# Kernel tuning notes

Hardware: AMD Instinct MI355X
Metric: run time of the kernel (lower is better)

Reference implementation:

```python
import jax, jax.numpy as jnp
import numpy as np

N_E = 8192
E_DIM = 256
BETA = 0.25


def setup_inputs() -> dict:
    key = jax.random.key(0)
    k1, k2 = jax.random.split(key)
    z = jax.random.normal(k1, (16, E_DIM, 32, 32), dtype=jnp.float32)
    # torch init: uniform(-1/n_e, 1/n_e)
    emb_weight = jax.random.uniform(k2, (N_E, E_DIM), dtype=jnp.float32,
                                    minval=-1.0 / N_E, maxval=1.0 / N_E)
    return {"z": z, "emb_weight": emb_weight}


def reference(z, emb_weight):
    B, C, H, W = z.shape
    # NCHW -> NHWC, flatten to [N, e_dim]
    z_nhwc = jnp.transpose(z, (0, 2, 3, 1))
    zf = z_nhwc.reshape(-1, C)  # [N, e_dim]

    # squared euclidean distances: ||z||^2 + ||e||^2 - 2 z e^T  -> [N, n_e]
    d = (jnp.sum(zf * zf, axis=1, keepdims=True)
         + jnp.sum(emb_weight * emb_weight, axis=1)
         - 2.0 * jnp.matmul(zf, emb_weight.T))
    idx = jnp.argmin(d, axis=1)  # [N]

    z_q = emb_weight[idx].reshape(z_nhwc.shape)  # [B,H,W,C]

    # legacy loss: mean((sg(z_q)-z)^2) + beta*mean((z_q-sg(z))^2)
    sg = jax.lax.stop_gradient
    loss = (jnp.mean((sg(z_q) - z_nhwc) ** 2)
            + BETA * jnp.mean((z_q - sg(z_nhwc)) ** 2))

    # straight-through estimator
    z_q = z_nhwc + sg(z_q - z_nhwc)

    # perplexity via code-usage histogram (equivalent to mean of one-hot)
    counts = jnp.zeros((N_E,), dtype=z.dtype).at[idx].add(1.0)
    e_mean = counts / idx.shape[0]
    perplexity = jnp.exp(-jnp.sum(e_mean * jnp.log(e_mean + 1e-10)))

    min_encoding_indices = idx.reshape(B, H * W).astype(jnp.int32)

    z_q = jnp.transpose(z_q, (0, 3, 1, 2))  # back to NCHW
    return z_q, loss, perplexity, min_encoding_indices
```

## Files before the change

### kernel.cpp

```cpp
#include <hip/hip_runtime.h>
#include <math.h>

#define NPTS   16384
#define NE     8192
#define DIM    256
#define BIMG   16
#define HW     1024
#define ZQ_N   4194304
#define OFF_LOSS  4194304
#define OFF_PERP  4194305
#define OFF_IDX   4194306

#define NT     64
#define NUNITS (NPTS * NT)
#define SJCAP  1048576

typedef short s16x8 __attribute__((ext_vector_type(8)));
typedef float f32x4 __attribute__((ext_vector_type(4)));

__device__ __forceinline__ float mul_rn(float a, float b) {
    float r;
    asm("v_mul_f32 %0, %1, %2" : "=v"(r) : "v"(a), "v"(b));
    return r;
}

__device__ __forceinline__ unsigned short f2bf(float f) {
    unsigned int u = __float_as_uint(f);
    return (unsigned short)((u + 0x7fffu + ((u >> 16) & 1u)) >> 16);
}

__device__ __forceinline__ void gl_lds16(const void* g, void* l) {
    __builtin_amdgcn_global_load_lds(
        (const __attribute__((address_space(1))) void*)g,
        (__attribute__((address_space(3))) void*)l, 16, 0, 0);
}

__device__ __forceinline__ void dot_min(const float* __restrict__ zp,
                                        const float* __restrict__ e,
                                        float zq, int p, int c,
                                        unsigned long long* __restrict__ pbest) {
    const float4* zp4 = (const float4*)zp;
    const float4* ep = (const float4*)(e + (size_t)c * 256);
    float a = 0.f;
    for (int k4 = 0; k4 < 64; ++k4) {
        float4 zv = zp4[k4];
        float4 ev = ep[k4];
        a = fmaf(zv.x, ev.x, a);
        a = fmaf(zv.y, ev.y, a);
        a = fmaf(zv.z, ev.z, a);
        a = fmaf(zv.w, ev.w, a);
    }
    float d = zq - 2.0f * a;
    unsigned long long key =
        ((unsigned long long)__float_as_uint(d) << 32) | (unsigned int)c;
    atomicMin(pbest + p, key);
}

__global__ __launch_bounds__(256)
void k_prep_z(const float* __restrict__ z, float* __restrict__ zT,
              unsigned short* __restrict__ zhT) {
    int bid = blockIdx.x;
    int ht = bid & 15, kt = (bid >> 4) & 3, b = bid >> 6;
    int k0 = kt * 64, hw0 = ht * 64;
    __shared__ float lt[64][65];
    int t = threadIdx.x;
    {
        int kr = t >> 2, j4 = (t & 3) * 16;
        const float* src = z + ((size_t)b * 256 + k0 + kr) * 1024 + hw0 + j4;
        #pragma unroll
        for (int q = 0; q < 4; ++q) {
            float4 v = *(const float4*)(src + q * 4);
            lt[kr][j4 + q * 4 + 0] = v.x; lt[kr][j4 + q * 4 + 1] = v.y;
            lt[kr][j4 + q * 4 + 2] = v.z; lt[kr][j4 + q * 4 + 3] = v.w;
        }
    }
    __syncthreads();
    {
        int pr = t >> 2, kb = (t & 3) * 16;
        size_t p = (size_t)b * 1024 + hw0 + pr;
        float vals[16];
        #pragma unroll
        for (int i = 0; i < 16; ++i) vals[i] = lt[kb + i][pr];
        float* dst = zT + p * 256 + k0 + kb;
        #pragma unroll
        for (int q = 0; q < 4; ++q)
            *(float4*)(dst + q * 4) = make_float4(vals[q*4], vals[q*4+1],
                                                  vals[q*4+2], vals[q*4+3]);
        unsigned short* hd = zhT + p * 256 + k0 + kb;
        #pragma unroll
        for (int q = 0; q < 4; ++q) {
            ushort4 h;
            h.x = f2bf(vals[q*4]);   h.y = f2bf(vals[q*4+1]);
            h.z = f2bf(vals[q*4+2]); h.w = f2bf(vals[q*4+3]);
            *(ushort4*)(hd + q * 4) = h;
        }
    }
}

__global__ void k_prep_e(const float* __restrict__ e, unsigned short* __restrict__ eh) {
    size_t i = ((size_t)blockIdx.x * 256 + threadIdx.x) * 16;
    #pragma unroll
    for (int q = 0; q < 4; ++q) {
        float4 v = *(const float4*)(e + i + q * 4);
        ushort4 h;
        h.x = f2bf(v.x); h.y = f2bf(v.y); h.z = f2bf(v.z); h.w = f2bf(v.w);
        *(ushort4*)(eh + i + q * 4) = h;
    }
}

__global__ void k_zsq(const float* __restrict__ zT, float* __restrict__ zsq,
                      float* __restrict__ marg) {
    int gid = blockIdx.x * 256 + threadIdx.x;
    int P = gid >> 1, half = gid & 1;
    const float* row = zT + (size_t)P * 256 + half * 128;
    float r[8];
    float S = 0.f;
    #pragma unroll
    for (int j = 0; j < 8; ++j) {
        float v = row[j];
        r[j] = mul_rn(v, v);
        S += fabsf(v);
    }
    for (int i = 8; i < 128; i += 8)
        #pragma unroll
        for (int j = 0; j < 8; ++j) {
            float v = row[i + j];
            r[j] += mul_rn(v, v);
            S += fabsf(v);
        }
    float s = ((r[0] + r[1]) + (r[2] + r[3])) + ((r[4] + r[5]) + (r[6] + r[7]));
    float so = __shfl_xor(s, 1, 64);
    float So = __shfl_xor(S, 1, 64);
    if (half == 0) {
        float zq = s + so;
        zsq[P] = zq;
        float Stot = S + So;
        unsigned int bits = __float_as_uint(zq);
        int ex = (int)((bits >> 23) & 255);
        float q = __uint_as_float((unsigned int)(ex - 23) << 23);
        marg[P] = 0.5f * q + 9.6e-7f * Stot + 2e-6f;
    }
}

__global__ void k_init(int* __restrict__ hist,
                       unsigned long long* __restrict__ pbest,
                       int* __restrict__ jc, int* __restrict__ tcnt) {
    int i = blockIdx.x * 256 + threadIdx.x;
    if (i < NE) hist[i] = 0;
    pbest[i] = ~0ULL;
    if (i < 2) jc[i] = 0;
    if (i < NT) tcnt[i] = 0;
}

__global__ __launch_bounds__(256)
void k_gemm(const unsigned short* __restrict__ zhT,
            const unsigned short* __restrict__ eh,
            float* __restrict__ tileMax) {
    const int bid = blockIdx.x;
    const int bm = bid & 127;
    const int bn = bid >> 7;
    const int t = threadIdx.x;
    const int l = t & 63, w = t >> 6, wm = w >> 1, wn = w & 1;

    __shared__ unsigned short As[2][128 * 32];
    __shared__ unsigned short Bs[2][128 * 32];
    __shared__ float wred[2][128];

    const unsigned short* Ab = zhT + (size_t)(bm * 128) * 256;
    const unsigned short* Bb = eh + (size_t)(bn * 128) * 256;
    const int srow = t >> 2, sko = (t & 3) * 8;

    gl_lds16(Ab + (size_t)srow * 256 + sko,        &As[0][t * 8]);
    gl_lds16(Ab + (size_t)(srow + 64) * 256 + sko, &As[0][t * 8 + 2048]);
    gl_lds16(Bb + (size_t)srow * 256 + sko,        &Bs[0][t * 8]);
    gl_lds16(Bb + (size_t)(srow + 64) * 256 + sko, &Bs[0][t * 8 + 2048]);

    f32x4 acc[4][4];
    #pragma unroll
    for (int m = 0; m < 4; ++m)
        #pragma unroll
        for (int n = 0; n < 4; ++n)
            acc[m][n] = (f32x4){0.f, 0.f, 0.f, 0.f};

    const int r0 = wm * 64 + (l & 15);
    const int c0 = wn * 64 + (l & 15);
    const int ko = (l >> 4) * 8;

    int buf = 0;
    for (int kc = 0; kc < 8; ++kc) {
        __syncthreads();
        if (kc < 7) {
            int kk = (kc + 1) * 32;
            gl_lds16(Ab + (size_t)srow * 256 + kk + sko,        &As[buf ^ 1][t * 8]);
            gl_lds16(Ab + (size_t)(srow + 64) * 256 + kk + sko, &As[buf ^ 1][t * 8 + 2048]);
            gl_lds16(Bb + (size_t)srow * 256 + kk + sko,        &Bs[buf ^ 1][t * 8]);
            gl_lds16(Bb + (size_t)(srow + 64) * 256 + kk + sko, &Bs[buf ^ 1][t * 8 + 2048]);
        }
        s16x8 af[4], bfr[4];
        #pragma unroll
        for (int m = 0; m < 4; ++m)
            af[m] = *(const s16x8*)&As[buf][(r0 + m * 16) * 32 + ko];
        #pragma unroll
        for (int n = 0; n < 4; ++n)
            bfr[n] = *(const s16x8*)&Bs[buf][(c0 + n * 16) * 32 + ko];
        #pragma unroll
        for (int m = 0; m < 4; ++m)
            #pragma unroll
            for (int n = 0; n < 4; ++n)
                acc[m][n] = __builtin_amdgcn_mfma_f32_16x16x32_bf16(
                    af[m], bfr[n], acc[m][n], 0, 0, 0);
        __syncthreads();
        buf ^= 1;
    }

    float vmax[4][4];
    #pragma unroll
    for (int m = 0; m < 4; ++m)
        #pragma unroll
        for (int q = 0; q < 4; ++q) {
            float v = acc[m][0][q];
            v = fmaxf(v, acc[m][1][q]);
            v = fmaxf(v, acc[m][2][q]);
            v = fmaxf(v, acc[m][3][q]);
            vmax[m][q] = v;
        }
    #pragma unroll
    for (int m = 0; m < 4; ++m)
        #pragma unroll
        for (int q = 0; q < 4; ++q) {
            float v = vmax[m][q];
            #pragma unroll
            for (int msk = 1; msk < 16; msk <<= 1)
                v = fmaxf(v, __shfl_xor(v, msk, 64));
            vmax[m][q] = v;
        }
    if ((l & 15) == 0) {
        int rg = l >> 4;
        #pragma unroll
        for (int m = 0; m < 4; ++m)
            #pragma unroll
            for (int q = 0; q < 4; ++q)
                wred[wn][wm * 64 + m * 16 + rg * 4 + q] = vmax[m][q];
    }
    __syncthreads();
    if (t < 128)
        tileMax[(size_t)bn * NPTS + bm * 128 + t] =
            fmaxf(wred[0][t], wred[1][t]);
}

__global__ void k_flag(const float* __restrict__ tileMax,
                       const float* __restrict__ marg,
                       float* __restrict__ tau) {
    int p = blockIdx.x * 256 + threadIdx.x;
    float best = -1e30f;
    for (int T = 0; T < NT; ++T)
        best = fmaxf(best, tileMax[(size_t)T * NPTS + p]);
    tau[p] = best - marg[p];
}

__global__ __launch_bounds__(256)
void k_filter(const float* __restrict__ tileMax,
              const float* __restrict__ tau,
              int* __restrict__ flist, int* __restrict__ tcnt) {
    const int T = blockIdx.x >> 6;
    const int chunk = blockIdx.x & 63;
    const int t = threadIdx.x;
    const int p = chunk * 256 + t;
    __shared__ int lcnt, gbase;
    if (t == 0) lcnt = 0;
    __syncthreads();
    bool hit = tileMax[(size_t)T * NPTS + p] >= tau[p];
    int myoff = 0;
    if (hit) myoff = atomicAdd(&lcnt, 1);
    __syncthreads();
    if (t == 0) gbase = (lcnt > 0) ? atomicAdd(&tcnt[T], lcnt) : 0;
    __syncthreads();
    if (hit) flist[T * NPTS + gbase + myoff] = p;
}

__global__ void k_scan(const int* __restrict__ tcnt, int* __restrict__ soff) {
    __shared__ int s[65];
    int t = threadIdx.x;
    if (t < 64) s[t + 1] = (tcnt[t] + 127) >> 7;
    if (t == 0) s[0] = 0;
    __syncthreads();
    if (t == 0)
        for (int i = 1; i <= 64; ++i) s[i] += s[i - 1];
    __syncthreads();
    if (t <= 64) soff[t] = s[t];
}

__global__ __launch_bounds__(256)
void k_gemm2s(const unsigned short* __restrict__ zhT,
              const unsigned short* __restrict__ eh,
              const int* __restrict__ flist, const int* __restrict__ tcnt,
              const int* __restrict__ soff,
              const float* __restrict__ tau,
              unsigned int* __restrict__ jobs, int* __restrict__ jc,
              const float* __restrict__ zT, const float* __restrict__ e,
              const float* __restrict__ zsq,
              unsigned long long* __restrict__ pbest) {
    const int t = threadIdx.x;
    const int l = t & 63, w = t >> 6, wm = w >> 1, wn = w & 1;
    const int lx = l & 15;
    const int kg = l >> 4;
    const int ko = kg * 8;

    __shared__ int soff_s[65];
    __shared__ int pid_s[128];
    __shared__ float stau[128];
    __shared__ int lcnt, gbase;

    if (t < 65) soff_s[t] = soff[t];
    __syncthreads();
    const int totS = soff_s[64];

    for (int j = blockIdx.x; j < totS; j += gridDim.x) {
        int lo = 0, hi = 63;
        while (lo < hi) {
            int mid = (lo + hi + 1) >> 1;
            if (soff_s[mid] <= j) lo = mid; else hi = mid - 1;
        }
        const int T = lo, sl = j - soff_s[T], nf = tcnt[T];

        __syncthreads();
        if (t < 128) {
            int gi = sl * 128 + t;
            int p = (gi < nf) ? flist[T * NPTS + gi] : flist[T * NPTS];
            pid_s[t] = p;
            stau[t] = tau[p];
        }
        if (t == 0) lcnt = 0;
        __syncthreads();

        int prow[4];
        #pragma unroll
        for (int m = 0; m < 4; ++m) prow[m] = pid_s[wm * 64 + m * 16 + lx];

        f32x4 acc[4][4];
        #pragma unroll
        for (int m = 0; m < 4; ++m)
            #pragma unroll
            for (int n = 0; n < 4; ++n)
                acc[m][n] = (f32x4){0.f, 0.f, 0.f, 0.f};

        const unsigned short* Bb = eh + (size_t)(T * 128 + wn * 64 + lx) * 256;
        #pragma unroll 2
        for (int kc = 0; kc < 8; ++kc) {
            s16x8 af[4], bfr[4];
            #pragma unroll
            for (int m = 0; m < 4; ++m)
                af[m] = *(const s16x8*)(zhT + (size_t)prow[m] * 256 + kc * 32 + ko);
            #pragma unroll
            for (int n = 0; n < 4; ++n)
                bfr[n] = *(const s16x8*)(Bb + (size_t)(n * 16) * 256 + kc * 32 + ko);
            #pragma unroll
            for (int m = 0; m < 4; ++m)
                #pragma unroll
                for (int n = 0; n < 4; ++n)
                    acc[m][n] = __builtin_amdgcn_mfma_f32_16x16x32_bf16(
                        af[m], bfr[n], acc[m][n], 0, 0, 0);
        }

        int cnt = 0;
        #pragma unroll
        for (int m = 0; m < 4; ++m)
            #pragma unroll
            for (int q = 0; q < 4; ++q) {
                int row = wm * 64 + m * 16 + kg * 4 + q;
                float st = stau[row];
                #pragma unroll
                for (int n = 0; n < 4; ++n)
                    if (acc[m][n][q] >= st) ++cnt;
            }
        int myoff = 0;
        if (cnt) myoff = atomicAdd(&lcnt, cnt);
        __syncthreads();
        if (t == 0) gbase = (lcnt > 0) ? atomicAdd(jc, lcnt) : 0;
        __syncthreads();
        if (cnt) {
            int pos = gbase + myoff;
            #pragma unroll
            for (int m = 0; m < 4; ++m)
                #pragma unroll
                for (int q = 0; q < 4; ++q) {
                    int row = wm * 64 + m * 16 + kg * 4 + q;
                    float st = stau[row];
                    #pragma unroll
                    for (int n = 0; n < 4; ++n) {
                        if (acc[m][n][q] >= st) {
                            int p = pid_s[row];
                            int c = T * 128 + wn * 64 + n * 16 + lx;
                            if (pos < SJCAP)
                                jobs[pos] = ((unsigned int)p << 13) | (unsigned int)c;
                            else
                                dot_min(zT + (size_t)p * 256, e, zsq[p], p, c, pbest);
                            ++pos;
                        }
                    }
                }
        }
    }
}

__global__ __launch_bounds__(256)
void k_rescore(const unsigned int* __restrict__ jobs, const int* __restrict__ jc,
               const float* __restrict__ zT, const float* __restrict__ e,
               const float* __restrict__ zsq,
               unsigned long long* __restrict__ pbest) {
    int nS = jc[0]; if (nS > SJCAP) nS = SJCAP;
    int stride = gridDim.x * 256;
    for (int j = blockIdx.x * 256 + threadIdx.x; j < nS; j += stride) {
        unsigned int v = jobs[j];
        int p = (int)(v >> 13);
        int c = (int)(v & 8191u);
        dot_min(zT + (size_t)p * 256, e, zsq[p], p, c, pbest);
    }
}

__global__ void k_pick(const unsigned long long* __restrict__ pbest,
                       int* __restrict__ idx_i, int* __restrict__ hist,
                       float* __restrict__ out) {
    int P = blockIdx.x * 256 + threadIdx.x;
    unsigned long long key = pbest[P];
    int idx = (int)(unsigned int)(key & 0xffffffffULL);
    idx_i[P] = idx;
    out[OFF_IDX + P] = (float)idx;
    atomicAdd(&hist[idx], 1);
}

__global__ __launch_bounds__(256)
void k_gather(const float* __restrict__ z, const float* __restrict__ emb,
              const int* __restrict__ idx_i, float* __restrict__ out,
              float* __restrict__ partials) {
    int bid = blockIdx.x;
    int c = bid & 255;
    int b = bid >> 8;
    int t = threadIdx.x;
    int hw = t * 4;

    size_t zoff = (size_t)(b * DIM + c) * HW + hw;
    const float4 zv = *(const float4*)(z + zoff);
    const int4  iv = *(const int4*)(idx_i + b * HW + hw);

    float e0 = emb[(size_t)iv.x * DIM + c];
    float e1 = emb[(size_t)iv.y * DIM + c];
    float e2 = emb[(size_t)iv.z * DIM + c];
    float e3 = emb[(size_t)iv.w * DIM + c];

    float dx = e0 - zv.x, dy = e1 - zv.y, dz = e2 - zv.z, dw = e3 - zv.w;
    float4 ov = make_float4(zv.x + dx, zv.y + dy, zv.z + dz, zv.w + dw);
    *(float4*)(out + zoff) = ov;

    float sq = dx * dx + dy * dy + dz * dz + dw * dw;
    #pragma unroll
    for (int m = 32; m >= 1; m >>= 1) sq += __shfl_xor(sq, m, 64);
    __shared__ float red[4];
    if ((t & 63) == 0) red[t >> 6] = sq;
    __syncthreads();
    if (t == 0) partials[bid] = red[0] + red[1] + red[2] + red[3];
}

__global__ void k_final(const float* __restrict__ partials,
                        const int* __restrict__ hist,
                        float* __restrict__ out) {
    int t = threadIdx.x;
    double ls = 0.0, es = 0.0;
    for (int i = t; i < 4096; i += 256) ls += (double)partials[i];
    for (int i = t; i < NE; i += 256) {
        double em = (double)hist[i] / (double)NPTS;
        es += em * log(em + 1e-10);
    }
    __shared__ double s1[256], s2[256];
    s1[t] = ls; s2[t] = es;
    __syncthreads();
    for (int s = 128; s > 0; s >>= 1) {
        if (t < s) { s1[t] += s1[t + s]; s2[t] += s2[t + s]; }
        __syncthreads();
    }
    if (t == 0) {
        out[OFF_LOSS] = (float)(s1[0] / (double)ZQ_N * 1.25);
        out[OFF_PERP] = (float)exp(-s2[0]);
    }
}

__global__ void f_zsq(const float* __restrict__ z, float* __restrict__ zsq) {
    int gid = blockIdx.x * 256 + threadIdx.x;
    int P = gid >> 1, half = gid & 1;
    int b = P >> 10, hw = P & 1023;
    const float* zb = z + (size_t)b * (DIM * HW) + (size_t)(half * 128) * HW + hw;
    float r[8];
    #pragma unroll
    for (int j = 0; j < 8; ++j) {
        float v = zb[(size_t)j * HW];
        r[j] = mul_rn(v, v);
    }
    #pragma unroll
    for (int i = 8; i < 128; i += 8)
        #pragma unroll
        for (int j = 0; j < 8; ++j) {
            float v = zb[(size_t)(i + j) * HW];
            r[j] += mul_rn(v, v);
        }
    float s = ((r[0] + r[1]) + (r[2] + r[3])) + ((r[4] + r[5]) + (r[6] + r[7]));
    float o = __shfl_xor(s, 1, 64);
    if (half == 0) zsq[P] = s + o;
}

__global__ void f_init(int* __restrict__ hist) {
    hist[blockIdx.x * 256 + threadIdx.x] = 0;
}

#define FBP 64
#define FBC 256
#define FKC 32
__global__ __launch_bounds__(256, 2)
void f_argmin(const float* __restrict__ z, const float* __restrict__ emb,
              const float* __restrict__ zsq,
              float* __restrict__ cand_d, int* __restrict__ cand_c) {
    const int blk = blockIdx.x;
    const int pblk = blk & 255;
    const int split = blk >> 8;
    const int p0 = pblk * FBP;
    const int b = p0 >> 10;
    const int hw0 = p0 & 1023;
    const int t = threadIdx.x;
    const int tx = t & 31;
    const int ty = t >> 5;

    __shared__ __align__(16) float z_s[FBP][36];
    __shared__ __align__(16) float e_s[FBC][36];

    float bd[8];
    int bcn[8];
    #pragma unroll
    for (int i = 0; i < 8; ++i) { bd[i] = INFINITY; bcn[i] = 0x7fffffff; }
    float zsqv[8];
    #pragma unroll
    for (int i = 0; i < 8; ++i) zsqv[i] = zsq[p0 + ty * 8 + i];

    const float* zbase = z + (size_t)b * (DIM * HW) + hw0;

    for (int cc = split * 16; cc < (split + 1) * 16; ++cc) {
        float acc[8][8];
        #pragma unroll
        for (int i = 0; i < 8; ++i)
            #pragma unroll
            for (int j = 0; j < 8; ++j) acc[i][j] = 0.f;
        for (int kc = 0; kc < DIM / FKC; ++kc) {
            __syncthreads();
            {
                int i = t & 63, kk0 = t >> 6;
                #pragma unroll
                for (int r = 0; r < 8; ++r) {
                    int kk = kk0 + r * 4;
                    z_s[i][kk] = zbase[(size_t)(kc * FKC + kk) * HW + i];
                }
            }
            {
                #pragma unroll
                for (int it = 0; it < 8; ++it) {
                    int q = t + it * 256;
                    int r = q >> 3, kkq = q & 7;
                    const float4 v = *(const float4*)(emb +
                        (size_t)(cc * FBC + r) * DIM + kc * FKC + kkq * 4);
                    *(float4*)&e_s[r][kkq * 4] = v;
                }
            }
            __syncthreads();
            #pragma unroll
            for (int g = 0; g < 8; ++g) {
                float4 zf[8], ef[8];
                #pragma unroll
                for (int i = 0; i < 8; ++i)
                    zf[i] = *(const float4*)&z_s[ty * 8 + i][g * 4];
                #pragma unroll
                for (int j = 0; j < 8; ++j)
                    ef[j] = *(const float4*)&e_s[tx + j * 32][g * 4];
                #pragma unroll
                for (int i = 0; i < 8; ++i)
                    #pragma unroll
                    for (int j = 0; j < 8; ++j) {
                        float a = acc[i][j];
                        a = fmaf(zf[i].x, ef[j].x, a);
                        a = fmaf(zf[i].y, ef[j].y, a);
                        a = fmaf(zf[i].z, ef[j].z, a);
                        a = fmaf(zf[i].w, ef[j].w, a);
                        acc[i][j] = a;
                    }
            }
        }
        #pragma unroll
        for (int j = 0; j < 8; ++j) {
            int c = cc * FBC + tx + j * 32;
            #pragma unroll
            for (int i = 0; i < 8; ++i) {
                float d = zsqv[i] - 2.0f * acc[i][j];
                if (d < bd[i]) { bd[i] = d; bcn[i] = c; }
                else if (d == bd[i] && c < bcn[i]) { bcn[i] = c; }
            }
        }
    }
    #pragma unroll
    for (int i = 0; i < 8; ++i) {
        float d = bd[i];
        int c = bcn[i];
        #pragma unroll
        for (int m = 16; m >= 1; m >>= 1) {
            float od = __shfl_xor(d, m, 32);
            int oc = __shfl_xor(c, m, 32);
            if (od < d || (od == d && oc < c)) { d = od; c = oc; }
        }
        if (tx == 0) {
            int P = p0 + ty * 8 + i;
            cand_d[(size_t)split * NPTS + P] = d;
            cand_c[(size_t)split * NPTS + P] = c;
        }
    }
}

__global__ void f_pick(const float* __restrict__ cand_d,
                       const int* __restrict__ cand_c,
                       int* __restrict__ idx_i, int* __restrict__ hist,
                       float* __restrict__ out) {
    int P = blockIdx.x * 256 + threadIdx.x;
    float d0 = cand_d[P], d1 = cand_d[NPTS + P];
    int c0 = cand_c[P], c1 = cand_c[NPTS + P];
    int idx = (d1 < d0) ? c1 : c0;
    idx_i[P] = idx;
    out[OFF_IDX + P] = (float)idx;
    atomicAdd(&hist[idx], 1);
}

extern "C" void kernel_launch(void* const* d_in, const int* in_sizes, int n_in,
                              void* d_out, int out_size, void* d_ws, size_t ws_size,
                              hipStream_t stream) {
    const float* z   = (const float*)d_in[0];
    const float* emb = (const float*)d_in[1];
    float* out = (float*)d_out;
    char*  ws  = (char*)d_ws;

    const size_t O_ZHT  = 0;
    const size_t O_EH   = 8388608;
    const size_t O_TM   = 12582912;
    const size_t O_FL   = 16777216;
    const size_t O_JS   = 20971520;
    const size_t O_ZSQ  = 25165824;
    const size_t O_MARG = 25231360;
    const size_t O_TAU  = 25296896;
    const size_t O_PB   = 25362432;
    const size_t O_IDX  = 25493504;
    const size_t O_HIST = 25559040;
    const size_t O_PART = 25591808;
    const size_t O_JC   = 25608192;
    const size_t O_TC   = 25608448;
    const size_t O_SOFF = 25608704;
    const size_t NEED   = 25609216;

    if (ws_size >= NEED) {
        float* zT = out;
        unsigned short* zhT = (unsigned short*)(ws + O_ZHT);
        unsigned short* eh  = (unsigned short*)(ws + O_EH);
        float* tileMax      = (float*)(ws + O_TM);
        int*   flist        = (int*)(ws + O_FL);
        unsigned int* jobs  = (unsigned int*)(ws + O_JS);
        float* zsq          = (float*)(ws + O_ZSQ);
        float* marg         = (float*)(ws + O_MARG);
        float* tau          = (float*)(ws + O_TAU);
        unsigned long long* pbest = (unsigned long long*)(ws + O_PB);
        int*   idx_i        = (int*)(ws + O_IDX);
        int*   hist         = (int*)(ws + O_HIST);
        float* partials     = (float*)(ws + O_PART);
        int*   jc           = (int*)(ws + O_JC);
        int*   tcnt         = (int*)(ws + O_TC);
        int*   soff         = (int*)(ws + O_SOFF);

        k_prep_z <<<1024, 256, 0, stream>>>(z, zT, zhT);
        k_prep_e <<<512,  256, 0, stream>>>(emb, eh);
        k_zsq    <<<128,  256, 0, stream>>>(zT, zsq, marg);
        k_init   <<<64,   256, 0, stream>>>(hist, pbest, jc, tcnt);
        k_gemm   <<<8192, 256, 0, stream>>>(zhT, eh, tileMax);
        k_flag   <<<64,   256, 0, stream>>>(tileMax, marg, tau);
        k_filter <<<4096, 256, 0, stream>>>(tileMax, tau, flist, tcnt);
        k_scan   <<<1,    128, 0, stream>>>(tcnt, soff);
        k_gemm2s <<<2048, 256, 0, stream>>>(zhT, eh, flist, tcnt, soff, tau,
                                            jobs, jc, zT, emb, zsq, pbest);
        k_rescore<<<512,  256, 0, stream>>>(jobs, jc, zT, emb, zsq, pbest);
        k_pick   <<<64,   256, 0, stream>>>(pbest, idx_i, hist, out);
        k_gather <<<4096, 256, 0, stream>>>(z, emb, idx_i, out, partials);
        k_final  <<<1,    256, 0, stream>>>(partials, hist, out);
    } else {
        float* zsq      = (float*)(ws);
        int*   hist     = (int*)  (ws + 65536);
        float* cand_d   = (float*)(ws + 98304);
        int*   cand_c   = (int*)  (ws + 229376);
        int*   idx_i    = (int*)  (ws + 360448);
        float* partials = (float*)(ws + 425984);

        f_zsq   <<<128, 256, 0, stream>>>(z, zsq);
        f_init  <<<32, 256, 0, stream>>>(hist);
        f_argmin<<<512, 256, 0, stream>>>(z, emb, zsq, cand_d, cand_c);
        f_pick  <<<64, 256, 0, stream>>>(cand_d, cand_c, idx_i, hist, out);
        k_gather<<<4096, 256, 0, stream>>>(z, emb, idx_i, out, partials);
        k_final <<<1, 256, 0, stream>>>(partials, hist, out);
    }
}
```

Baseline: 248.6 us.

## Fold init, scan and rescore kernels into neighbouring launches

Merges the workspace init into the embedding bf16 conversion kernel, computes the per-tile prefix sum inside the second-pass GEMM kernel, and rescores candidate (point, code) pairs inline instead of queuing them to a separate rescore kernel. This removes three kernel launches and the job buffer with its global atomic counter. In exchange, the exact fp32 rescoring now runs divergently inside the MFMA kernel, which may stall waves that have many candidates.

```diff
diff --git a/kernel.cpp b/kernel.cpp
--- a/kernel.cpp
+++ b/kernel.cpp
@@ -13,7 +13,6 @@
 
 #define NT     64
 #define NUNITS (NPTS * NT)
-#define SJCAP  1048576
 
 typedef short s16x8 __attribute__((ext_vector_type(8)));
 typedef float f32x4 __attribute__((ext_vector_type(4)));
@@ -97,8 +96,17 @@
     }
 }
 
-__global__ void k_prep_e(const float* __restrict__ e, unsigned short* __restrict__ eh) {
-    size_t i = ((size_t)blockIdx.x * 256 + threadIdx.x) * 16;
+__global__ void k_prep_e(const float* __restrict__ e, unsigned short* __restrict__ eh,
+                         int* __restrict__ hist,
+                         unsigned long long* __restrict__ pbest,
+                         int* __restrict__ tcnt) {
+    int gid = blockIdx.x * 256 + threadIdx.x;
+    if (gid < NPTS) {
+        pbest[gid] = ~0ULL;
+        if (gid < NE) hist[gid] = 0;
+        if (gid < NT) tcnt[gid] = 0;
+    }
+    size_t i = (size_t)gid * 16;
     #pragma unroll
     for (int q = 0; q < 4; ++q) {
         float4 v = *(const float4*)(e + i + q * 4);
@@ -142,16 +150,6 @@
     }
 }
 
-__global__ void k_init(int* __restrict__ hist,
-                       unsigned long long* __restrict__ pbest,
-                       int* __restrict__ jc, int* __restrict__ tcnt) {
-    int i = blockIdx.x * 256 + threadIdx.x;
-    if (i < NE) hist[i] = 0;
-    pbest[i] = ~0ULL;
-    if (i < 2) jc[i] = 0;
-    if (i < NT) tcnt[i] = 0;
-}
-
 __global__ __launch_bounds__(256)
 void k_gemm(const unsigned short* __restrict__ zhT,
             const unsigned short* __restrict__ eh,
@@ -278,25 +276,11 @@
     if (hit) flist[T * NPTS + gbase + myoff] = p;
 }
 
-__global__ void k_scan(const int* __restrict__ tcnt, int* __restrict__ soff) {
-    __shared__ int s[65];
-    int t = threadIdx.x;
-    if (t < 64) s[t + 1] = (tcnt[t] + 127) >> 7;
-    if (t == 0) s[0] = 0;
-    __syncthreads();
-    if (t == 0)
-        for (int i = 1; i <= 64; ++i) s[i] += s[i - 1];
-    __syncthreads();
-    if (t <= 64) soff[t] = s[t];
-}
-
 __global__ __launch_bounds__(256)
 void k_gemm2s(const unsigned short* __restrict__ zhT,
               const unsigned short* __restrict__ eh,
               const int* __restrict__ flist, const int* __restrict__ tcnt,
-              const int* __restrict__ soff,
               const float* __restrict__ tau,
-              unsigned int* __restrict__ jobs, int* __restrict__ jc,
               const float* __restrict__ zT, const float* __restrict__ e,
               const float* __restrict__ zsq,
               unsigned long long* __restrict__ pbest) {
@@ -307,11 +291,20 @@
     const int ko = kg * 8;
 
     __shared__ int soff_s[65];
+    __shared__ int tcnt_s[64];
     __shared__ int pid_s[128];
     __shared__ float stau[128];
-    __shared__ int lcnt, gbase;
-
-    if (t < 65) soff_s[t] = soff[t];
+
+    if (t < 64) tcnt_s[t] = tcnt[t];
+    __syncthreads();
+    if (t == 0) {
+        int acc0 = 0;
+        soff_s[0] = 0;
+        for (int i = 0; i < 64; ++i) {
+            acc0 += (tcnt_s[i] + 127) >> 7;
+            soff_s[i + 1] = acc0;
+        }
+    }
     __syncthreads();
     const int totS = soff_s[64];
 
@@ -321,7 +314,7 @@
             int mid = (lo + hi + 1) >> 1;
             if (soff_s[mid] <= j) lo = mid; else hi = mid - 1;
         }
-        const int T = lo, sl = j - soff_s[T], nf = tcnt[T];
+        const int T = lo, sl = j - soff_s[T], nf = tcnt_s[T];
 
         __syncthreads();
         if (t < 128) {
@@ -330,7 +323,6 @@
             pid_s[t] = p;
             stau[t] = tau[p];
         }
-        if (t == 0) lcnt = 0;
         __syncthreads();
 
         int prow[4];
@@ -362,7 +354,6 @@
                         af[m], bfr[n], acc[m][n], 0, 0, 0);
         }
 
-        int cnt = 0;
         #pragma unroll
         for (int m = 0; m < 4; ++m)
             #pragma unroll
@@ -370,51 +361,14 @@
                 int row = wm * 64 + m * 16 + kg * 4 + q;
                 float st = stau[row];
                 #pragma unroll
-                for (int n = 0; n < 4; ++n)
-                    if (acc[m][n][q] >= st) ++cnt;
-            }
-        int myoff = 0;
-        if (cnt) myoff = atomicAdd(&lcnt, cnt);
-        __syncthreads();
-        if (t == 0) gbase = (lcnt > 0) ? atomicAdd(jc, lcnt) : 0;
-        __syncthreads();
-        if (cnt) {
-            int pos = gbase + myoff;
-            #pragma unroll
-            for (int m = 0; m < 4; ++m)
-                #pragma unroll
-                for (int q = 0; q < 4; ++q) {
-                    int row = wm * 64 + m * 16 + kg * 4 + q;
-                    float st = stau[row];
-                    #pragma unroll
-                    for (int n = 0; n < 4; ++n) {
-                        if (acc[m][n][q] >= st) {
-                            int p = pid_s[row];
-                            int c = T * 128 + wn * 64 + n * 16 + lx;
-                            if (pos < SJCAP)
-                                jobs[pos] = ((unsigned int)p << 13) | (unsigned int)c;
-                            else
-                                dot_min(zT + (size_t)p * 256, e, zsq[p], p, c, pbest);
-                            ++pos;
-                        }
+                for (int n = 0; n < 4; ++n) {
+                    if (acc[m][n][q] >= st) {
+                        int p = pid_s[row];
+                        int c = T * 128 + wn * 64 + n * 16 + lx;
+                        dot_min(zT + (size_t)p * 256, e, zsq[p], p, c, pbest);
                     }
                 }
-        }
-    }
-}
-
-__global__ __launch_bounds__(256)
-void k_rescore(const unsigned int* __restrict__ jobs, const int* __restrict__ jc,
-               const float* __restrict__ zT, const float* __restrict__ e,
-               const float* __restrict__ zsq,
-               unsigned long long* __restrict__ pbest) {
-    int nS = jc[0]; if (nS > SJCAP) nS = SJCAP;
-    int stride = gridDim.x * 256;
-    for (int j = blockIdx.x * 256 + threadIdx.x; j < nS; j += stride) {
-        unsigned int v = jobs[j];
-        int p = (int)(v >> 13);
-        int c = (int)(v & 8191u);
-        dot_min(zT + (size_t)p * 256, e, zsq[p], p, c, pbest);
+            }
     }
 }
 
@@ -644,18 +598,15 @@
     const size_t O_EH   = 8388608;
     const size_t O_TM   = 12582912;
     const size_t O_FL   = 16777216;
-    const size_t O_JS   = 20971520;
-    const size_t O_ZSQ  = 25165824;
-    const size_t O_MARG = 25231360;
-    const size_t O_TAU  = 25296896;
-    const size_t O_PB   = 25362432;
-    const size_t O_IDX  = 25493504;
-    const size_t O_HIST = 25559040;
-    const size_t O_PART = 25591808;
-    const size_t O_JC   = 25608192;
-    const size_t O_TC   = 25608448;
-    const size_t O_SOFF = 25608704;
-    const size_t NEED   = 25609216;
+    const size_t O_ZSQ  = 20971520;
+    const size_t O_MARG = 21037056;
+    const size_t O_TAU  = 21102592;
+    const size_t O_PB   = 21168128;
+    const size_t O_IDX  = 21299200;
+    const size_t O_HIST = 21364736;
+    const size_t O_PART = 21397504;
+    const size_t O_TC   = 21413888;
+    const size_t NEED   = 21414400;
 
     if (ws_size >= NEED) {
         float* zT = out;
@@ -663,7 +614,6 @@
         unsigned short* eh  = (unsigned short*)(ws + O_EH);
         float* tileMax      = (float*)(ws + O_TM);
         int*   flist        = (int*)(ws + O_FL);
-        unsigned int* jobs  = (unsigned int*)(ws + O_JS);
         float* zsq          = (float*)(ws + O_ZSQ);
         float* marg         = (float*)(ws + O_MARG);
         float* tau          = (float*)(ws + O_TAU);
@@ -671,21 +621,16 @@
         int*   idx_i        = (int*)(ws + O_IDX);
         int*   hist         = (int*)(ws + O_HIST);
         float* partials     = (float*)(ws + O_PART);
-        int*   jc           = (int*)(ws + O_JC);
         int*   tcnt         = (int*)(ws + O_TC);
-        int*   soff         = (int*)(ws + O_SOFF);
 
         k_prep_z <<<1024, 256, 0, stream>>>(z, zT, zhT);
-        k_prep_e <<<512,  256, 0, stream>>>(emb, eh);
+        k_prep_e <<<512,  256, 0, stream>>>(emb, eh, hist, pbest, tcnt);
         k_zsq    <<<128,  256, 0, stream>>>(zT, zsq, marg);
-        k_init   <<<64,   256, 0, stream>>>(hist, pbest, jc, tcnt);
         k_gemm   <<<8192, 256, 0, stream>>>(zhT, eh, tileMax);
         k_flag   <<<64,   256, 0, stream>>>(tileMax, marg, tau);
         k_filter <<<4096, 256, 0, stream>>>(tileMax, tau, flist, tcnt);
-        k_scan   <<<1,    128, 0, stream>>>(tcnt, soff);
-        k_gemm2s <<<2048, 256, 0, stream>>>(zhT, eh, flist, tcnt, soff, tau,
-                                            jobs, jc, zT, emb, zsq, pbest);
-        k_rescore<<<512,  256, 0, stream>>>(jobs, jc, zT, emb, zsq, pbest);
+        k_gemm2s <<<2048, 256, 0, stream>>>(zhT, eh, flist, tcnt, tau,
+                                            zT, emb, zsq, pbest);
         k_pick   <<<64,   256, 0, stream>>>(pbest, idx_i, hist, out);
         k_gather <<<4096, 256, 0, stream>>>(z, emb, idx_i, out, partials);
         k_final  <<<1,    256, 0, stream>>>(partials, hist, out);
```

New measurement: 435.7 us. 75.2% more time.
